# Kernel tuning notes

Hardware: AMD Instinct MI355X
Metric: run time of the kernel (lower is better)

## Reference

```python
import jax, jax.numpy as jnp
import numpy as np

ALPHA = 0.2  # LeakyReLU negative slope
N, F_IN, F_OUT = 8192, 512, 64
NEG_BIG = -9e15


def setup_inputs() -> dict:
    key = jax.random.key(0)
    k1, k2, k3, k4 = jax.random.split(key, 4)
    h = jax.random.normal(k1, (N, F_IN), dtype=jnp.float32)
    # xavier_uniform with gain 1.414
    lim_w = 1.414 * np.sqrt(6.0 / (F_IN + F_OUT))
    W = jax.random.uniform(k2, (F_IN, F_OUT), dtype=jnp.float32, minval=-lim_w, maxval=lim_w)
    lim_a = 1.414 * np.sqrt(6.0 / (2 * F_OUT + 1))
    a = jax.random.uniform(k3, (2 * F_OUT, 1), dtype=jnp.float32, minval=-lim_a, maxval=lim_a)
    adj = jax.random.randint(k4, (N, N), 0, 2, dtype=jnp.int32)
    return {"h": h, "W": W, "a": a, "adj": adj}


def reference(h, W, a, adj):
    Wh = h @ W                                  # [N, F_OUT]
    f_out = Wh.shape[1]
    a1 = a[:f_out, 0]                            # source half of attention vector
    a2 = a[f_out:, 0]                            # target half
    # e_ij = LeakyReLU(Wh_i . a1 + Wh_j . a2); equals cat([Wh_i, Wh_j]) @ a
    e = jax.nn.leaky_relu(jnp.matmul(Wh, a1)[:, None] + jnp.matmul(Wh, a2)[None, :], ALPHA)  # [N, N]
    attention = jnp.where(adj > 0, e, NEG_BIG)
    attention = jax.nn.softmax(attention, axis=1)
    # dropout is a no-op at inference (training=False)
    h_prime = attention @ Wh                     # [N, F_OUT]
    return jax.nn.elu(h_prime)                   # concat=True -> ELU
```

## Files before the change

### kernel.cpp

```cpp
#include <hip/hip_runtime.h>
#include <hip/hip_bf16.h>


typedef _Float16 f16;
typedef _Float16 f16x2 __attribute__((ext_vector_type(2)));
typedef _Float16 f16x4 __attribute__((ext_vector_type(4)));
typedef _Float16 f16x8 __attribute__((ext_vector_type(8)));
typedef float f32x4 __attribute__((ext_vector_type(4)));
typedef int   i32x4 __attribute__((ext_vector_type(4)));

#define GAT_N 8192
#define GAT_FIN 512
#define GAT_FOUT 64
#define GAT_ALPHA 0.2f

__global__ void k0_wtrans(const float* __restrict__ W, f16* __restrict__ WT) {
    int idx = blockIdx.x * blockDim.x + threadIdx.x;
    int k = idx >> 6, c = idx & 63;
    WT[c * GAT_FIN + k] = (f16)W[idx];
}

__global__ __launch_bounds__(256) void k1_gemm(const float* __restrict__ h,
        const f16* __restrict__ WT, const float* __restrict__ a,
        f16* __restrict__ WhT, float* __restrict__ s1, float* __restrict__ s2) {
    __shared__ float pacc[4][4][64][4];
    __shared__ float s1red[4][16], s2red[4][16];

    int tid = threadIdx.x;
    int w = tid >> 6, lane = tid & 63;
    int l15 = lane & 15, quad = lane >> 4;
    int rb = blockIdx.x * 16;
    size_t arow = (size_t)(rb + l15) * GAT_FIN;

    f32x4 acc[4] = {};
#pragma unroll
    for (int ks = 0; ks < 4; ks++) {
        int kb = w * 128 + ks * 32 + quad * 8;
        const float4* hp = (const float4*)(h + arow + kb);
        float4 h0 = hp[0], h1 = hp[1];
        f16x8 af = { (f16)h0.x, (f16)h0.y, (f16)h0.z, (f16)h0.w,
                     (f16)h1.x, (f16)h1.y, (f16)h1.z, (f16)h1.w };
#pragma unroll
        for (int t = 0; t < 4; t++) {
            f16x8 bf = *(const f16x8*)(WT + (t * 16 + l15) * GAT_FIN + kb);
            acc[t] = __builtin_amdgcn_mfma_f32_16x16x32_f16(af, bf, acc[t], 0, 0, 0);
        }
    }
#pragma unroll
    for (int t = 0; t < 4; t++)
        *(f32x4*)&pacc[w][t][lane][0] = acc[t];
    __syncthreads();

    float a1v = a[w * 16 + l15];
    float a2v = a[GAT_FOUT + w * 16 + l15];
    float vreg[4];
#pragma unroll
    for (int reg = 0; reg < 4; reg++) {
        float v = 0.f;
#pragma unroll
        for (int ww = 0; ww < 4; ww++) v += pacc[ww][w][lane][reg];
        vreg[reg] = v;
    }
    f16x4 pk = { (f16)vreg[0], (f16)vreg[1], (f16)vreg[2], (f16)vreg[3] };
    *(f16x4*)(WhT + (size_t)(w * 16 + l15) * GAT_N + rb + quad * 4) = pk;

#pragma unroll
    for (int reg = 0; reg < 4; reg++) {
        float c1 = vreg[reg] * a1v, c2 = vreg[reg] * a2v;
#pragma unroll
        for (int off = 1; off < 16; off <<= 1) {
            c1 += __shfl_xor(c1, off);
            c2 += __shfl_xor(c2, off);
        }
        if (l15 == 0) { s1red[w][quad * 4 + reg] = c1; s2red[w][quad * 4 + reg] = c2; }
    }
    __syncthreads();
    if (tid < 16) {
        float t1 = 0.f, t2 = 0.f;
#pragma unroll
        for (int ww = 0; ww < 4; ww++) { t1 += s1red[ww][tid]; t2 += s2red[ww][tid]; }
        s1[rb + tid] = t1;
        s2[rb + tid] = t2;
    }
}

__global__ __launch_bounds__(512, 4) void k3_attn(const int* __restrict__ adj,
        const f16* __restrict__ WhT, const float* __restrict__ s1,
        const float* __restrict__ s2, float* __restrict__ out) {
    __shared__ __align__(16) char smem[2 * 16 * 520 * 2];
    f16* pbuf = (f16*)smem;
    float (*accbuf)[16][64] = (float (*)[16][64])smem;
    __shared__ float dbuf2[16];
    __shared__ float mred[8];

    int tid = threadIdx.x;
    int w = tid >> 6, lane = tid & 63;
    int l15 = lane & 15, quad = lane >> 4;
    int hhalf = lane >> 5, q = lane & 31;
    int rb = blockIdx.x * 16;
    int r = 2 * w + hhalf;

    float m = -1e30f;
    for (int i = tid; i < GAT_N; i += 512) m = fmaxf(m, s2[i]);
#pragma unroll
    for (int off = 32; off >= 1; off >>= 1) m = fmaxf(m, __shfl_xor(m, off));
    if (lane == 0) mred[w] = m;
    __syncthreads();
    float mxv = mred[0];
#pragma unroll
    for (int ww = 1; ww < 8; ww++) mxv = fmaxf(mxv, mred[ww]);

    float s1r = s1[rb + r];
    float cr = s1r + mxv;
    cr = fmaxf(cr, GAT_ALPHA * cr);
    const int* adjrow = adj + (size_t)(rb + r) * GAT_N;

    float dacc = 0.f;
    f32x4 acc[4] = {};
    i32x4  av[4];
    float4 sv[4];

    auto stage = [&](int bb) {
#pragma unroll
        for (int p = 0; p < 4; p++) {
            float svv[4] = { sv[p].x, sv[p].y, sv[p].z, sv[p].w };
            int base = (4 * p + (q >> 3)) * 520 + ((q >> 1) & 3) * 128 + r * 8 + (q & 1) * 4;
            f16 pf[4];
#pragma unroll
            for (int j = 0; j < 4; j++) {
                float e = s1r + svv[j];
                e = fmaxf(e, GAT_ALPHA * e);
                float pv = __expf(e - cr);
                pv = (av[p][j] > 0) ? pv : 0.0f;
                dacc += pv;
                pf[j] = (f16)pv;
            }
            f16x2 lo = { pf[0], pf[1] }, hi = { pf[2], pf[3] };
            *(f16x2*)&pbuf[bb * 8320 + base]     = lo;
            *(f16x2*)&pbuf[bb * 8320 + base + 2] = hi;
        }
    };

#pragma unroll
    for (int p = 0; p < 4; p++) {
        int c0 = p * 128 + q * 4;
        av[p] = __builtin_nontemporal_load((const i32x4*)(adjrow + c0));
        sv[p] = *(const float4*)(s2 + c0);
    }
    stage(0);
    __syncthreads();

    for (int rd = 0; rd < 16; rd++) {
        int b = rd & 1;
        if (rd < 15) {
#pragma unroll
            for (int p = 0; p < 4; p++) {
                int c0 = (rd + 1) * 512 + p * 128 + q * 4;
                av[p] = __builtin_nontemporal_load((const i32x4*)(adjrow + c0));
                sv[p] = *(const float4*)(s2 + c0);
            }
        }
#pragma unroll
        for (int sl = 0; sl < 2; sl++) {
            int s_loc = 2 * w + sl;
            f16x8 af = *(const f16x8*)&pbuf[b * 8320 + s_loc * 520 + lane * 8];
            int kb = rd * 512 + s_loc * 32 + quad * 8;
#pragma unroll
            for (int t = 0; t < 4; t++) {
                f16x8 bf = *(const f16x8*)(WhT + (size_t)(t * 16 + l15) * GAT_N + kb);
                acc[t] = __builtin_amdgcn_mfma_f32_16x16x32_f16(af, bf, acc[t], 0, 0, 0);
            }
        }
        if (rd < 15) stage(1 - b);
        __syncthreads();
    }

#pragma unroll
    for (int t = 0; t < 4; t++)
#pragma unroll
        for (int reg = 0; reg < 4; reg++)
            accbuf[w][quad * 4 + reg][t * 16 + l15] = acc[t][reg];
#pragma unroll
    for (int off = 16; off >= 1; off >>= 1) dacc += __shfl_xor(dacc, off);
    if (q == 0) dbuf2[r] = dacc;
    __syncthreads();

    for (int o = tid; o < 16 * 64; o += 512) {
        int rr = o >> 6, c = o & 63;
        float num = 0.f;
#pragma unroll
        for (int ww = 0; ww < 8; ww++) num += accbuf[ww][rr][c];
        float hp = num / dbuf2[rr];
        out[(size_t)(rb + rr) * GAT_FOUT + c] = hp > 0.f ? hp : expm1f(hp);
    }
}

extern "C" void kernel_launch(void* const* d_in, const int* in_sizes, int n_in,
                              void* d_out, int out_size, void* d_ws, size_t ws_size,
                              hipStream_t stream) {
    const float* h   = (const float*)d_in[0];
    const float* W   = (const float*)d_in[1];
    const float* a   = (const float*)d_in[2];
    const int*   adj = (const int*)d_in[3];
    float* out = (float*)d_out;

    char* ws = (char*)d_ws;
    f16*   WT  = (f16*)ws;
    f16*   WhT = (f16*)(ws + 65536);
    float* s1  = (float*)(ws + 65536 + 1048576);
    float* s2  = (float*)(ws + 65536 + 1048576 + 32768);

    k0_wtrans<<<128, 256, 0, stream>>>(W, WT);
    k1_gemm<<<512, 256, 0, stream>>>(h, WT, a, WhT, s1, s2);
    k3_attn<<<512, 512, 0, stream>>>(adj, WhT, s1, s2, out);
}
```

Before: 407.8 us.

## Give each wave a private column slice to drop per-round block barriers

Changes the attention kernel's work split. Each wave now computes softmax numerators for all 16 rows over its own 64-column slice per round and writes them to a private LDS tile. The old scheme had each wave produce two full rows into a shared double-buffered tile, which needed a __syncthreads every round. Denominators are reduced per wave and combined at the end. This removes the 16 per-round block barriers and shrinks LDS use, but the adj loads change shape to 16-lane row segments, which may reduce coalescing.

```diff
diff --git a/kernel.cpp b/kernel.cpp
--- a/kernel.cpp
+++ b/kernel.cpp
@@ -87,18 +87,17 @@
 __global__ __launch_bounds__(512, 4) void k3_attn(const int* __restrict__ adj,
         const f16* __restrict__ WhT, const float* __restrict__ s1,
         const float* __restrict__ s2, float* __restrict__ out) {
-    __shared__ __align__(16) char smem[2 * 16 * 520 * 2];
+    __shared__ __align__(16) char smem[16 * 64 * 8 * 4];
     f16* pbuf = (f16*)smem;
     float (*accbuf)[16][64] = (float (*)[16][64])smem;
-    __shared__ float dbuf2[16];
+    __shared__ float dred[8][16];
     __shared__ float mred[8];
 
     int tid = threadIdx.x;
     int w = tid >> 6, lane = tid & 63;
     int l15 = lane & 15, quad = lane >> 4;
-    int hhalf = lane >> 5, q = lane & 31;
     int rb = blockIdx.x * 16;
-    int r = 2 * w + hhalf;
+    f16* pw = pbuf + w * (16 * 72);
 
     float m = -1e30f;
     for (int i = tid; i < GAT_N; i += 512) m = fmaxf(m, s2[i]);
@@ -110,87 +109,95 @@
 #pragma unroll
     for (int ww = 1; ww < 8; ww++) mxv = fmaxf(mxv, mred[ww]);
 
-    float s1r = s1[rb + r];
-    float cr = s1r + mxv;
-    cr = fmaxf(cr, GAT_ALPHA * cr);
-    const int* adjrow = adj + (size_t)(rb + r) * GAT_N;
-
-    float dacc = 0.f;
+    float s1v[4], crv[4];
+#pragma unroll
+    for (int i = 0; i < 4; i++) {
+        float s = s1[rb + 4 * i + quad];
+        s1v[i] = s;
+        float c = s + mxv;
+        crv[i] = fmaxf(c, GAT_ALPHA * c);
+    }
+
     f32x4 acc[4] = {};
+    float daccv[4] = { 0.f, 0.f, 0.f, 0.f };
     i32x4  av[4];
-    float4 sv[4];
-
-    auto stage = [&](int bb) {
-#pragma unroll
-        for (int p = 0; p < 4; p++) {
-            float svv[4] = { sv[p].x, sv[p].y, sv[p].z, sv[p].w };
-            int base = (4 * p + (q >> 3)) * 520 + ((q >> 1) & 3) * 128 + r * 8 + (q & 1) * 4;
+    float4 sv;
+
+    int C0 = w * 64;
+#pragma unroll
+    for (int i = 0; i < 4; i++)
+        av[i] = __builtin_nontemporal_load(
+            (const i32x4*)(adj + (size_t)(rb + 4 * i + quad) * GAT_N + C0 + l15 * 4));
+    sv = *(const float4*)(s2 + C0 + l15 * 4);
+
+    for (int ci = 0; ci < 16; ci++) {
+        i32x4 avn[4];
+        float4 svn;
+        int C1 = C0 + 512;
+        if (ci < 15) {
+#pragma unroll
+            for (int i = 0; i < 4; i++)
+                avn[i] = __builtin_nontemporal_load(
+                    (const i32x4*)(adj + (size_t)(rb + 4 * i + quad) * GAT_N + C1 + l15 * 4));
+            svn = *(const float4*)(s2 + C1 + l15 * 4);
+        }
+
+        float svv[4] = { sv.x, sv.y, sv.z, sv.w };
+#pragma unroll
+        for (int i = 0; i < 4; i++) {
             f16 pf[4];
 #pragma unroll
             for (int j = 0; j < 4; j++) {
-                float e = s1r + svv[j];
+                float e = s1v[i] + svv[j];
                 e = fmaxf(e, GAT_ALPHA * e);
-                float pv = __expf(e - cr);
-                pv = (av[p][j] > 0) ? pv : 0.0f;
-                dacc += pv;
+                float pv = __expf(e - crv[i]);
+                pv = (av[i][j] > 0) ? pv : 0.0f;
+                daccv[i] += pv;
                 pf[j] = (f16)pv;
             }
-            f16x2 lo = { pf[0], pf[1] }, hi = { pf[2], pf[3] };
-            *(f16x2*)&pbuf[bb * 8320 + base]     = lo;
-            *(f16x2*)&pbuf[bb * 8320 + base + 2] = hi;
-        }
-    };
-
-#pragma unroll
-    for (int p = 0; p < 4; p++) {
-        int c0 = p * 128 + q * 4;
-        av[p] = __builtin_nontemporal_load((const i32x4*)(adjrow + c0));
-        sv[p] = *(const float4*)(s2 + c0);
-    }
-    stage(0);
-    __syncthreads();
-
-    for (int rd = 0; rd < 16; rd++) {
-        int b = rd & 1;
-        if (rd < 15) {
-#pragma unroll
-            for (int p = 0; p < 4; p++) {
-                int c0 = (rd + 1) * 512 + p * 128 + q * 4;
-                av[p] = __builtin_nontemporal_load((const i32x4*)(adjrow + c0));
-                sv[p] = *(const float4*)(s2 + c0);
-            }
-        }
+            f16x4 pk = { pf[0], pf[1], pf[2], pf[3] };
+            *(f16x4*)&pw[(4 * i + quad) * 72 + l15 * 4] = pk;
+        }
+
 #pragma unroll
         for (int sl = 0; sl < 2; sl++) {
-            int s_loc = 2 * w + sl;
-            f16x8 af = *(const f16x8*)&pbuf[b * 8320 + s_loc * 520 + lane * 8];
-            int kb = rd * 512 + s_loc * 32 + quad * 8;
+            f16x8 af = *(const f16x8*)&pw[l15 * 72 + sl * 32 + quad * 8];
+            int kb = C0 + sl * 32 + quad * 8;
 #pragma unroll
             for (int t = 0; t < 4; t++) {
                 f16x8 bf = *(const f16x8*)(WhT + (size_t)(t * 16 + l15) * GAT_N + kb);
                 acc[t] = __builtin_amdgcn_mfma_f32_16x16x32_f16(af, bf, acc[t], 0, 0, 0);
             }
         }
-        if (rd < 15) stage(1 - b);
-        __syncthreads();
-    }
-
+#pragma unroll
+        for (int i = 0; i < 4; i++) av[i] = avn[i];
+        sv = svn;
+        C0 = C1;
+    }
+
+#pragma unroll
+    for (int i = 0; i < 4; i++) {
+#pragma unroll
+        for (int off = 1; off < 16; off <<= 1) daccv[i] += __shfl_xor(daccv[i], off);
+    }
+    __syncthreads();
+    if (l15 == 0) {
+#pragma unroll
+        for (int i = 0; i < 4; i++) dred[w][4 * i + quad] = daccv[i];
+    }
 #pragma unroll
     for (int t = 0; t < 4; t++)
 #pragma unroll
         for (int reg = 0; reg < 4; reg++)
             accbuf[w][quad * 4 + reg][t * 16 + l15] = acc[t][reg];
-#pragma unroll
-    for (int off = 16; off >= 1; off >>= 1) dacc += __shfl_xor(dacc, off);
-    if (q == 0) dbuf2[r] = dacc;
     __syncthreads();
 
     for (int o = tid; o < 16 * 64; o += 512) {
         int rr = o >> 6, c = o & 63;
-        float num = 0.f;
-#pragma unroll
-        for (int ww = 0; ww < 8; ww++) num += accbuf[ww][rr][c];
-        float hp = num / dbuf2[rr];
+        float num = 0.f, den = 0.f;
+#pragma unroll
+        for (int ww = 0; ww < 8; ww++) { num += accbuf[ww][rr][c]; den += dred[ww][rr]; }
+        float hp = num / den;
         out[(size_t)(rb + rr) * GAT_FOUT + c] = hp > 0.f ? hp : expm1f(hp);
     }
 }
```

New measurement: 410.7 us. About the same (+0.7%).
